# Optimization experiments

Hardware: AMD Instinct MI355X
Metric: run time of the kernel (lower is better)

## Reference

```python
import jax, jax.numpy as jnp
import numpy as np

B, C, H, W_SP = 32, 128, 56, 56
OC, K, STRIDE, PAD = 256, 3, 1, 1


def setup_inputs() -> dict:
    key = jax.random.key(0)
    k1, k2, k3 = jax.random.split(key, 3)
    x = jax.random.normal(k1, (B, C, H, W_SP), dtype=jnp.float32)
    # nn.Linear weight: [out_features, in_features] = [OC, C*K*K]
    W = jax.random.normal(k2, (OC, C * K * K), dtype=jnp.float32) * 0.02
    b = jax.random.normal(k3, (OC,), dtype=jnp.float32) * 0.02
    return {"x": x, "W": W, "b": b}


def reference(x, W, b):
    # The torch module does im2col (unfold+permute+reshape) then Linear.
    # Patch layout after view/permute is (C, kh, kw) flattened, so the
    # Linear weight reshaped to [OC, C, K, K] is exactly an OIHW conv
    # kernel; direct convolution computes identical math without
    # materializing the im2col tensor.
    kernel = W.reshape(OC, C, K, K)
    out = jax.lax.conv_general_dilated(
        x, kernel,
        window_strides=(STRIDE, STRIDE),
        padding=[(PAD, PAD), (PAD, PAD)],
        dimension_numbers=("NCHW", "OIHW", "NCHW"),
    )
    return out + b[None, :, None, None]
```

## Files before the change

kernel.cpp:

```cpp
#include <hip/hip_runtime.h>
#include <hip/hip_bf16.h>
#include <stdint.h>

typedef unsigned short u16;
typedef unsigned int   u32;
typedef __bf16 bf16x8 __attribute__((ext_vector_type(8)));
typedef float  f32x4  __attribute__((ext_vector_type(4)));

#define BATCH 32
#define CIN   128
#define HH    56
#define WW    56
#define OC    256
#define HP    58
#define WP    58
#define PLANE  (HH*WW)
#define KDIM   1152
#define NKT    36

#define XPAD_ELEMS (BATCH*HP*WP*CIN)
#define W3_ELEMS   (OC*KDIM)

#define GLDS16(g, l) __builtin_amdgcn_global_load_lds( \
    (const __attribute__((address_space(1))) void*)(g), \
    (__attribute__((address_space(3))) void*)(l), 16, 0, 0)

__global__ void zero_border(uint4* __restrict__ xp4) {
    int i = blockIdx.x * 256 + threadIdx.x;
    if (i >= 64 * 928) return;
    int row = i / 928;
    int off = i - row * 928;
    int b = row >> 1;
    int h = (row & 1) ? (HP - 1) : 0;
    xp4[((size_t)(b * HP + h) * WP * CIN) / 8 + off] = (uint4){0, 0, 0, 0};
}

__global__ __launch_bounds__(256) void pad_tr(const float* __restrict__ x,
                                              u16* __restrict__ xpad) {
    __shared__ u16 T16[56 * 130];
    const int h = blockIdx.x;
    const int b = blockIdx.y;
    const int tid = threadIdx.x;

    const float* src = x + (size_t)b * CIN * PLANE + h * WW;
#pragma unroll
    for (int j = 0; j < 28; ++j) {
        int flat = j * 256 + tid;
        int c = flat / 56;
        int w = flat - c * 56;
        float v = src[(size_t)c * PLANE + w];
        __hip_bfloat16 bv = __float2bfloat16(v);
        T16[w * 130 + c] = *(u16*)&bv;
    }
    __syncthreads();

    const u32* T32 = (const u32*)T16;
    uint4* dst = (uint4*)(xpad + (size_t)(b * HP + h + 1) * WP * CIN);
#pragma unroll
    for (int j = 0; j < 4; ++j) {
        int g = j * 256 + tid;
        if (g < 928) {
            int wp = g >> 4, cq = g & 15;
            uint4 v = (uint4){0, 0, 0, 0};
            if (wp >= 1 && wp <= 56) {
                int w = wp - 1;
                v.x = T32[w * 65 + cq * 4 + 0];
                v.y = T32[w * 65 + cq * 4 + 1];
                v.z = T32[w * 65 + cq * 4 + 2];
                v.w = T32[w * 65 + cq * 4 + 3];
            }
            dst[g] = v;
        }
    }
}

__global__ void pack_w(const float* __restrict__ W, u16* __restrict__ w3) {
    int o = blockIdx.x * blockDim.x + threadIdx.x;
    if (o >= W3_ELEMS) return;
    int nt   = o / (NKT * 4096);
    int rem  = o - nt * (NKT * 4096);
    int kt   = rem / 4096;
    int rem2 = rem - kt * 4096;
    int ni   = rem2 >> 5;
    int ci   = rem2 & 31;
    int n = nt * 128 + ni;
    int r = kt >> 2;
    int c = ((kt & 3) << 5) + ci;
    float val = W[n * KDIM + c * 9 + r];
    __hip_bfloat16 bv = __float2bfloat16(val);
    w3[o] = *(u16*)&bv;
}

__global__ __launch_bounds__(256) void conv_main(
    const u16* __restrict__ xpad,
    const u16* __restrict__ w3,
    const float* __restrict__ bias,
    float* __restrict__ out)
{
    __shared__ __align__(16) u16 As[2][128 * 32];
    __shared__ __align__(16) u16 Bs[2][128 * 32];

    const int tid  = threadIdx.x;
    const int lane = tid & 63;
    const int wv   = tid >> 6;
    const int m0   = blockIdx.x * 128;
    const int nt   = blockIdx.y;

    const int srow = lane >> 2;
    const int sc   = lane & 3;
    size_t abase[2], bbase[2];
#pragma unroll
    for (int i = 0; i < 2; ++i) {
        int rowid = wv * 32 + i * 16 + srow;
        int q = (sc - ((rowid >> 1) & 3)) & 3;
        abase[i] = (size_t)rowid * 64 + q * 16;
        int m  = m0 + rowid;
        int bb = m / PLANE;
        int s  = m - bb * PLANE;
        int hh = s / WW;
        int ww = s - hh * WW;
        bbase[i] = ((size_t)((bb * HP + hh) * WP + ww) * CIN) * 2 + q * 16;
    }
    const char* w3t = (const char*)(w3 + (size_t)nt * (NKT * 4096));
    const char* xb  = (const char*)xpad;
    char* AsW[2] = { (char*)As[0] + wv * 2048, (char*)As[1] + wv * 2048 };
    char* BsW[2] = { (char*)Bs[0] + wv * 2048, (char*)Bs[1] + wv * 2048 };

    const int wn = wv >> 1, wm = wv & 1;
    const int l16 = lane & 15, quad = lane >> 4;

    int aoff[4], boff[4];
#pragma unroll
    for (int f = 0; f < 4; ++f) {
        int ra = wn * 64 + f * 16 + l16;
        aoff[f] = ra * 64 + ((quad + (ra >> 1)) & 3) * 16;
        int rb = wm * 64 + f * 16 + l16;
        boff[f] = rb * 64 + ((quad + (rb >> 1)) & 3) * 16;
    }

    f32x4 acc[4][4];
#pragma unroll
    for (int f = 0; f < 4; ++f) {
        f32x4 bv = *(const f32x4*)&bias[nt * 128 + wn * 64 + f * 16 + quad * 4];
#pragma unroll
        for (int g = 0; g < 4; ++g) acc[f][g] = bv;
    }

    auto issue = [&](int kt) {
        const int buf = kt & 1;
        const int r  = kt >> 2;
        const int cc = kt & 3;
        const int kh = r / 3;
        const int kw = r - kh * 3;
        const size_t xoff = ((size_t)(kh * WP + kw) * CIN + cc * 32) * 2;
#pragma unroll
        for (int i = 0; i < 2; ++i) {
            GLDS16(w3t + (size_t)kt * 8192 + abase[i], AsW[buf] + i * 1024);
            GLDS16(xb + bbase[i] + xoff,               BsW[buf] + i * 1024);
        }
    };

    issue(0);
#pragma unroll
    for (int kt = 0; kt < NKT; ++kt) {
        __syncthreads();
        if (kt + 1 < NKT) issue(kt + 1);

        const char* Ab = (const char*)As[kt & 1];
        const char* Bb = (const char*)Bs[kt & 1];
        bf16x8 af[4], bfr[4];
#pragma unroll
        for (int f = 0; f < 4; ++f)
            af[f] = *(const bf16x8*)(Ab + aoff[f]);
#pragma unroll
        for (int g = 0; g < 4; ++g)
            bfr[g] = *(const bf16x8*)(Bb + boff[g]);

#pragma unroll
        for (int f = 0; f < 4; ++f)
#pragma unroll
            for (int g = 0; g < 4; ++g)
                acc[f][g] = __builtin_amdgcn_mfma_f32_16x16x32_bf16(
                    af[f], bfr[g], acc[f][g], 0, 0, 0);
    }

    const int n0 = nt * 128 + wn * 64;
#pragma unroll
    for (int g = 0; g < 4; ++g) {
        const int mm = m0 + wm * 64 + g * 16 + l16;
        const int bb = mm / PLANE;
        const int ss = mm - bb * PLANE;
        float* obase = out + (size_t)bb * (OC * PLANE) + ss;
#pragma unroll
        for (int f = 0; f < 4; ++f) {
#pragma unroll
            for (int i = 0; i < 4; ++i) {
                const int n = n0 + f * 16 + quad * 4 + i;
                obase[(size_t)n * PLANE] = acc[f][g][i];
            }
        }
    }
}

extern "C" void kernel_launch(void* const* d_in, const int* in_sizes, int n_in,
                              void* d_out, int out_size, void* d_ws, size_t ws_size,
                              hipStream_t stream) {
    const float* x    = (const float*)d_in[0];
    const float* W    = (const float*)d_in[1];
    const float* bias = (const float*)d_in[2];
    float* out = (float*)d_out;

    u16* xpad = (u16*)d_ws;
    u16* w3   = xpad + XPAD_ELEMS;

    zero_border<<<232, 256, 0, stream>>>((uint4*)xpad);
    pad_tr<<<dim3(HH, BATCH), 256, 0, stream>>>(x, xpad);
    pack_w<<<(W3_ELEMS + 255) / 256, 256, 0, stream>>>(W, w3);

    dim3 grid(784, 2);
    conv_main<<<grid, 256, 0, stream>>>(xpad, w3, bias, out);
}
```

Measured before the change: 217.1 us.

## Enlarge conv GEMM tile to 256x256 with K=64 steps and staged ping-pong pipeline

The implicit-GEMM convolution moves from 128x128 tiles with K=32 steps to 256(M)x256(N) tiles with K=64 steps, using 8 waves per block and 392 blocks. The weight packing is rewritten into a matching swizzled layout. The main loop splits each K step into four MFMA quadrants, with interleaved async global-to-LDS staging, explicit barriers, waitcnt control and setprio, which should improve data reuse and overlap loads with compute. Block IDs are also remapped to spread tiles. The risks are higher register and LDS pressure and fewer blocks than the CU count for good occupancy.

```diff
diff --git a/kernel.cpp b/kernel.cpp
--- a/kernel.cpp
+++ b/kernel.cpp
@@ -16,7 +16,7 @@
 #define WP    58
 #define PLANE  (HH*WW)
 #define KDIM   1152
-#define NKT    36
+#define NT     18
 
 #define XPAD_ELEMS (BATCH*HP*WP*CIN)
 #define W3_ELEMS   (OC*KDIM)
@@ -77,127 +77,216 @@
 __global__ void pack_w(const float* __restrict__ W, u16* __restrict__ w3) {
     int o = blockIdx.x * blockDim.x + threadIdx.x;
     if (o >= W3_ELEMS) return;
-    int nt   = o / (NKT * 4096);
-    int rem  = o - nt * (NKT * 4096);
-    int kt   = rem / 4096;
-    int rem2 = rem - kt * 4096;
-    int ni   = rem2 >> 5;
-    int ci   = rem2 & 31;
-    int n = nt * 128 + ni;
-    int r = kt >> 2;
-    int c = ((kt & 3) << 5) + ci;
-    float val = W[n * KDIM + c * 9 + r];
+    int T   = o >> 14;
+    int rem = o & 16383;
+    int oc  = rem >> 6;
+    int kk  = rem & 63;
+    int p   = kk >> 3;
+    int e   = kk & 7;
+    int rot = ((oc & 127) >> 1) & 7;
+    int c64 = ((p - rot) & 7) * 8 + e;
+    int r   = T >> 1;
+    int c128 = (T & 1) * 64 + c64;
+    float val = W[oc * KDIM + c128 * 9 + r];
     __hip_bfloat16 bv = __float2bfloat16(val);
     w3[o] = *(u16*)&bv;
 }
 
-__global__ __launch_bounds__(256) void conv_main(
+__global__ __launch_bounds__(512, 2) void conv_main(
     const u16* __restrict__ xpad,
     const u16* __restrict__ w3,
     const float* __restrict__ bias,
     float* __restrict__ out)
 {
-    __shared__ __align__(16) u16 As[2][128 * 32];
-    __shared__ __align__(16) u16 Bs[2][128 * 32];
+    __shared__ __align__(16) u16 WL[2 * 2 * 128 * 64];
+    __shared__ __align__(16) u16 XL[2 * 2 * 128 * 64];
 
     const int tid  = threadIdx.x;
     const int lane = tid & 63;
     const int wv   = tid >> 6;
-    const int m0   = blockIdx.x * 128;
-    const int nt   = blockIdx.y;
-
-    const int srow = lane >> 2;
-    const int sc   = lane & 3;
-    size_t abase[2], bbase[2];
-#pragma unroll
-    for (int i = 0; i < 2; ++i) {
-        int rowid = wv * 32 + i * 16 + srow;
-        int q = (sc - ((rowid >> 1) & 3)) & 3;
-        abase[i] = (size_t)rowid * 64 + q * 16;
-        int m  = m0 + rowid;
-        int bb = m / PLANE;
-        int s  = m - bb * PLANE;
-        int hh = s / WW;
-        int ww = s - hh * WW;
-        bbase[i] = ((size_t)((bb * HP + hh) * WP + ww) * CIN) * 2 + q * 16;
-    }
-    const char* w3t = (const char*)(w3 + (size_t)nt * (NKT * 4096));
+    const int wm   = wv >> 2;
+    const int wn   = wv & 3;
+    const int l16  = lane & 15;
+    const int quad = lane >> 4;
+
+    const int bid  = blockIdx.x;
+    const int tile = (bid & 7) * 49 + (bid >> 3);
+    const int m0   = tile * 256;
+
+    const int srow8 = lane >> 3;
+    const int spos  = lane & 7;
+    size_t xsrc[2][2];
+#pragma unroll
+    for (int h = 0; h < 2; ++h)
+#pragma unroll
+        for (int i = 0; i < 2; ++i) {
+            int r  = (wv * 2 + i) * 8 + srow8;
+            int q  = (spos - ((r >> 1) & 7)) & 7;
+            int m  = m0 + h * 128 + r;
+            int b  = m / PLANE;
+            int s  = m - b * PLANE;
+            int hh = s / WW;
+            int ww = s - hh * WW;
+            xsrc[h][i] = ((size_t)((b * HP + hh) * WP + ww) * CIN) * 2 + (size_t)q * 16;
+        }
     const char* xb  = (const char*)xpad;
-    char* AsW[2] = { (char*)As[0] + wv * 2048, (char*)As[1] + wv * 2048 };
-    char* BsW[2] = { (char*)Bs[0] + wv * 2048, (char*)Bs[1] + wv * 2048 };
-
-    const int wn = wv >> 1, wm = wv & 1;
-    const int l16 = lane & 15, quad = lane >> 4;
-
-    int aoff[4], boff[4];
+    const char* w3b = (const char*)w3;
+    const int dstat     = wv * 2048;
+    const int wsrc_lane = wv * 2048 + lane * 16;
+
+    auto xkoff = [&](int kt) -> int {
+        int r9 = kt >> 1;
+        int kh = (r9 * 11) >> 5;
+        int kw = r9 - kh * 3;
+        return ((kh * WP + kw) * CIN + (kt & 1) * 64) * 2;
+    };
+    auto stageW = [&](int kt, int h) {
+        const char* src = w3b + (size_t)kt * 32768 + h * 16384 + wsrc_lane;
+        char* dst = (char*)WL + (kt & 1) * 32768 + h * 16384 + dstat;
+        GLDS16(src,        dst);
+        GLDS16(src + 1024, dst + 1024);
+    };
+    auto stageX = [&](int kt, int h, int xko) {
+        char* dst = (char*)XL + (kt & 1) * 32768 + h * 16384 + dstat;
+        GLDS16(xb + xsrc[h][0] + xko, dst);
+        GLDS16(xb + xsrc[h][1] + xko, dst + 1024);
+    };
+
+    int woff[2], xoff[4];
+#pragma unroll
+    for (int j = 0; j < 2; ++j) {
+        int r = wn * 32 + j * 16 + l16;
+        woff[j] = r * 128 + (((quad + (r >> 1)) & 7) << 4);
+    }
+#pragma unroll
+    for (int j = 0; j < 4; ++j) {
+        int r = wm * 64 + j * 16 + l16;
+        xoff[j] = r * 128 + (((quad + (r >> 1)) & 7) << 4);
+    }
+
+    f32x4 acc[4][8];
 #pragma unroll
     for (int f = 0; f < 4; ++f) {
-        int ra = wn * 64 + f * 16 + l16;
-        aoff[f] = ra * 64 + ((quad + (ra >> 1)) & 3) * 16;
-        int rb = wm * 64 + f * 16 + l16;
-        boff[f] = rb * 64 + ((quad + (rb >> 1)) & 3) * 16;
-    }
-
-    f32x4 acc[4][4];
-#pragma unroll
-    for (int f = 0; f < 4; ++f) {
-        f32x4 bv = *(const f32x4*)&bias[nt * 128 + wn * 64 + f * 16 + quad * 4];
-#pragma unroll
-        for (int g = 0; g < 4; ++g) acc[f][g] = bv;
-    }
-
-    auto issue = [&](int kt) {
-        const int buf = kt & 1;
-        const int r  = kt >> 2;
-        const int cc = kt & 3;
-        const int kh = r / 3;
-        const int kw = r - kh * 3;
-        const size_t xoff = ((size_t)(kh * WP + kw) * CIN + cc * 32) * 2;
-#pragma unroll
-        for (int i = 0; i < 2; ++i) {
-            GLDS16(w3t + (size_t)kt * 8192 + abase[i], AsW[buf] + i * 1024);
-            GLDS16(xb + bbase[i] + xoff,               BsW[buf] + i * 1024);
-        }
-    };
-
-    issue(0);
-#pragma unroll
-    for (int kt = 0; kt < NKT; ++kt) {
-        __syncthreads();
-        if (kt + 1 < NKT) issue(kt + 1);
-
-        const char* Ab = (const char*)As[kt & 1];
-        const char* Bb = (const char*)Bs[kt & 1];
-        bf16x8 af[4], bfr[4];
-#pragma unroll
-        for (int f = 0; f < 4; ++f)
-            af[f] = *(const bf16x8*)(Ab + aoff[f]);
-#pragma unroll
-        for (int g = 0; g < 4; ++g)
-            bfr[g] = *(const bf16x8*)(Bb + boff[g]);
-
-#pragma unroll
-        for (int f = 0; f < 4; ++f)
+        const int ob = (f >> 1) * 128 + wn * 32 + (f & 1) * 16 + quad * 4;
+        f32x4 bv = *(const f32x4*)&bias[ob];
+#pragma unroll
+        for (int g = 0; g < 8; ++g) acc[f][g] = bv;
+    }
+
+    stageW(0, 0); stageW(0, 1);
+    stageX(0, 0, xkoff(0)); stageX(0, 1, xkoff(0));
+    stageW(1, 0); stageX(1, 0, xkoff(1)); stageW(1, 1);
+    asm volatile("s_waitcnt vmcnt(6)" ::: "memory");
+    __builtin_amdgcn_sched_barrier(0);
+    __builtin_amdgcn_s_barrier();
+
+#pragma unroll 1
+    for (int kt = 0; kt < NT; ++kt) {
+        const char* Wb = (const char*)WL + (kt & 1) * 32768;
+        const char* Xb = (const char*)XL + (kt & 1) * 32768;
+        const bool st2 = (kt + 2 < NT);
+
+        bf16x8 wlo[2][2], xlo[4][2];
+#pragma unroll
+        for (int j = 0; j < 2; ++j) {
+            wlo[j][0] = *(const bf16x8*)(Wb + woff[j]);
+            wlo[j][1] = *(const bf16x8*)(Wb + (woff[j] ^ 64));
+        }
+#pragma unroll
+        for (int j = 0; j < 4; ++j) {
+            xlo[j][0] = *(const bf16x8*)(Xb + xoff[j]);
+            xlo[j][1] = *(const bf16x8*)(Xb + (xoff[j] ^ 64));
+        }
+        if (kt + 1 < NT) stageX(kt + 1, 1, xkoff(kt + 1));
+        __builtin_amdgcn_s_barrier();
+        asm volatile("s_waitcnt lgkmcnt(0)" ::: "memory");
+        __builtin_amdgcn_sched_barrier(0);
+        __builtin_amdgcn_s_setprio(1);
+#pragma unroll
+        for (int f = 0; f < 2; ++f)
 #pragma unroll
             for (int g = 0; g < 4; ++g)
-                acc[f][g] = __builtin_amdgcn_mfma_f32_16x16x32_bf16(
-                    af[f], bfr[g], acc[f][g], 0, 0, 0);
-    }
-
-    const int n0 = nt * 128 + wn * 64;
-#pragma unroll
-    for (int g = 0; g < 4; ++g) {
-        const int mm = m0 + wm * 64 + g * 16 + l16;
+#pragma unroll
+                for (int s = 0; s < 2; ++s)
+                    acc[f][g] = __builtin_amdgcn_mfma_f32_16x16x32_bf16(
+                        wlo[f][s], xlo[g][s], acc[f][g], 0, 0, 0);
+        __builtin_amdgcn_s_setprio(0);
+        __builtin_amdgcn_s_barrier();
+
+        bf16x8 whi[2][2];
+#pragma unroll
+        for (int j = 0; j < 2; ++j) {
+            whi[j][0] = *(const bf16x8*)(Wb + 16384 + woff[j]);
+            whi[j][1] = *(const bf16x8*)(Wb + 16384 + (woff[j] ^ 64));
+        }
+        if (st2) stageW(kt + 2, 0);
+        __builtin_amdgcn_s_barrier();
+        asm volatile("s_waitcnt lgkmcnt(0)" ::: "memory");
+        __builtin_amdgcn_sched_barrier(0);
+        __builtin_amdgcn_s_setprio(1);
+#pragma unroll
+        for (int f = 0; f < 2; ++f)
+#pragma unroll
+            for (int g = 0; g < 4; ++g)
+#pragma unroll
+                for (int s = 0; s < 2; ++s)
+                    acc[2 + f][g] = __builtin_amdgcn_mfma_f32_16x16x32_bf16(
+                        whi[f][s], xlo[g][s], acc[2 + f][g], 0, 0, 0);
+        __builtin_amdgcn_s_setprio(0);
+        __builtin_amdgcn_s_barrier();
+
+        bf16x8 xhi[4][2];
+#pragma unroll
+        for (int j = 0; j < 4; ++j) {
+            xhi[j][0] = *(const bf16x8*)(Xb + 16384 + xoff[j]);
+            xhi[j][1] = *(const bf16x8*)(Xb + 16384 + (xoff[j] ^ 64));
+        }
+        if (st2) stageX(kt + 2, 0, xkoff(kt + 2));
+        __builtin_amdgcn_s_barrier();
+        asm volatile("s_waitcnt lgkmcnt(0)" ::: "memory");
+        __builtin_amdgcn_sched_barrier(0);
+        __builtin_amdgcn_s_setprio(1);
+#pragma unroll
+        for (int f = 0; f < 2; ++f)
+#pragma unroll
+            for (int g = 0; g < 4; ++g)
+#pragma unroll
+                for (int s = 0; s < 2; ++s)
+                    acc[f][4 + g] = __builtin_amdgcn_mfma_f32_16x16x32_bf16(
+                        wlo[f][s], xhi[g][s], acc[f][4 + g], 0, 0, 0);
+        __builtin_amdgcn_s_setprio(0);
+        __builtin_amdgcn_s_barrier();
+
+        if (st2) stageW(kt + 2, 1);
+        __builtin_amdgcn_s_barrier();
+        __builtin_amdgcn_s_setprio(1);
+#pragma unroll
+        for (int f = 0; f < 2; ++f)
+#pragma unroll
+            for (int g = 0; g < 4; ++g)
+#pragma unroll
+                for (int s = 0; s < 2; ++s)
+                    acc[2 + f][4 + g] = __builtin_amdgcn_mfma_f32_16x16x32_bf16(
+                        whi[f][s], xhi[g][s], acc[2 + f][4 + g], 0, 0, 0);
+        __builtin_amdgcn_s_setprio(0);
+        if (kt < NT - 2) asm volatile("s_waitcnt vmcnt(6)" ::: "memory");
+        else             asm volatile("s_waitcnt vmcnt(0)" ::: "memory");
+        __builtin_amdgcn_sched_barrier(0);
+        __builtin_amdgcn_s_barrier();
+    }
+
+#pragma unroll
+    for (int g = 0; g < 8; ++g) {
+        const int mm = m0 + (g >> 2) * 128 + wm * 64 + (g & 3) * 16 + l16;
         const int bb = mm / PLANE;
         const int ss = mm - bb * PLANE;
         float* obase = out + (size_t)bb * (OC * PLANE) + ss;
 #pragma unroll
         for (int f = 0; f < 4; ++f) {
-#pragma unroll
-            for (int i = 0; i < 4; ++i) {
-                const int n = n0 + f * 16 + quad * 4 + i;
-                obase[(size_t)n * PLANE] = acc[f][g][i];
-            }
+            const int n = (f >> 1) * 128 + wn * 32 + (f & 1) * 16 + quad * 4;
+#pragma unroll
+            for (int i = 0; i < 4; ++i)
+                obase[(size_t)(n + i) * PLANE] = acc[f][g][i];
         }
     }
 }
@@ -217,6 +306,5 @@
     pad_tr<<<dim3(HH, BATCH), 256, 0, stream>>>(x, xpad);
     pack_w<<<(W3_ELEMS + 255) / 256, 256, 0, stream>>>(W, w3);
 
-    dim3 grid(784, 2);
-    conv_main<<<grid, 256, 0, stream>>>(xpad, w3, bias, out);
-}
+    conv_main<<<392, 512, 0, stream>>>(xpad, w3, bias, out);
+}
```

New measurement: 224.1 us. 1.03x slower.

## Compute all 256 output channels per block and remap tiles across XCDs

Applied to the files above, without the earlier changes.

The conv GEMM block tile grows from 128x128 to 256 output channels by 128 pixels, so each block loads the padded input tile once instead of twice across two channel-tile blocks. The weight pack layout is changed to pre-apply the LDS swizzle, tiles are remapped so neighbouring pixel tiles land on the same XCD, MFMA sections get raised wave priority, and the main loop is no longer unrolled. The pad/transpose kernel reads float2 pairs. Accumulators double to 128 floats per thread, which raises register pressure and may cost occupancy despite the launch-bounds hint.

```diff
diff --git a/kernel.cpp b/kernel.cpp
--- a/kernel.cpp
+++ b/kernel.cpp
@@ -16,7 +16,7 @@
 #define WP    58
 #define PLANE  (HH*WW)
 #define KDIM   1152
-#define NKT    36
+#define NT     36
 
 #define XPAD_ELEMS (BATCH*HP*WP*CIN)
 #define W3_ELEMS   (OC*KDIM)
@@ -44,13 +44,16 @@
 
     const float* src = x + (size_t)b * CIN * PLANE + h * WW;
 #pragma unroll
-    for (int j = 0; j < 28; ++j) {
+    for (int j = 0; j < 14; ++j) {
         int flat = j * 256 + tid;
-        int c = flat / 56;
-        int w = flat - c * 56;
-        float v = src[(size_t)c * PLANE + w];
-        __hip_bfloat16 bv = __float2bfloat16(v);
-        T16[w * 130 + c] = *(u16*)&bv;
+        int c  = flat / 28;
+        int wp = flat - c * 28;
+        int w  = wp * 2;
+        float2 v = *(const float2*)&src[(size_t)c * PLANE + w];
+        __hip_bfloat16 b0 = __float2bfloat16(v.x);
+        __hip_bfloat16 b1 = __float2bfloat16(v.y);
+        T16[w * 130 + c]       = *(u16*)&b0;
+        T16[(w + 1) * 130 + c] = *(u16*)&b1;
     }
     __syncthreads();
 
@@ -77,127 +80,135 @@
 __global__ void pack_w(const float* __restrict__ W, u16* __restrict__ w3) {
     int o = blockIdx.x * blockDim.x + threadIdx.x;
     if (o >= W3_ELEMS) return;
-    int nt   = o / (NKT * 4096);
-    int rem  = o - nt * (NKT * 4096);
-    int kt   = rem / 4096;
-    int rem2 = rem - kt * 4096;
-    int ni   = rem2 >> 5;
-    int ci   = rem2 & 31;
-    int n = nt * 128 + ni;
-    int r = kt >> 2;
-    int c = ((kt & 3) << 5) + ci;
-    float val = W[n * KDIM + c * 9 + r];
+    int T   = o >> 13;
+    int rem = o & 8191;
+    int oc  = rem >> 5;
+    int kk  = rem & 31;
+    int p   = kk >> 3;
+    int e   = kk & 7;
+    int rot = (oc >> 1) & 3;
+    int c32 = ((p - rot) & 3) * 8 + e;
+    int r   = T >> 2;
+    int c128 = (T & 3) * 32 + c32;
+    float val = W[oc * KDIM + c128 * 9 + r];
     __hip_bfloat16 bv = __float2bfloat16(val);
     w3[o] = *(u16*)&bv;
 }
 
-__global__ __launch_bounds__(256) void conv_main(
+__global__ __launch_bounds__(256, 2) void conv_main(
     const u16* __restrict__ xpad,
     const u16* __restrict__ w3,
     const float* __restrict__ bias,
     float* __restrict__ out)
 {
-    __shared__ __align__(16) u16 As[2][128 * 32];
-    __shared__ __align__(16) u16 Bs[2][128 * 32];
+    __shared__ __align__(16) u16 WL[2][256 * 32];
+    __shared__ __align__(16) u16 XL[2][128 * 32];
 
     const int tid  = threadIdx.x;
     const int lane = tid & 63;
     const int wv   = tid >> 6;
-    const int m0   = blockIdx.x * 128;
-    const int nt   = blockIdx.y;
-
-    const int srow = lane >> 2;
-    const int sc   = lane & 3;
-    size_t abase[2], bbase[2];
+    const int l16  = lane & 15;
+    const int quad = lane >> 4;
+
+    const int bid  = blockIdx.x;
+    const int tile = (bid & 7) * 98 + (bid >> 3);
+    const int m0   = tile * 128;
+
+    const int srow = tid >> 2;
+    const int spos = tid & 3;
+    size_t xsrc[2];
 #pragma unroll
     for (int i = 0; i < 2; ++i) {
-        int rowid = wv * 32 + i * 16 + srow;
-        int q = (sc - ((rowid >> 1) & 3)) & 3;
-        abase[i] = (size_t)rowid * 64 + q * 16;
-        int m  = m0 + rowid;
-        int bb = m / PLANE;
-        int s  = m - bb * PLANE;
+        int r  = i * 64 + srow;
+        int q  = (spos - ((r >> 1) & 3)) & 3;
+        int m  = m0 + r;
+        int b  = m / PLANE;
+        int s  = m - b * PLANE;
         int hh = s / WW;
         int ww = s - hh * WW;
-        bbase[i] = ((size_t)((bb * HP + hh) * WP + ww) * CIN) * 2 + q * 16;
-    }
-    const char* w3t = (const char*)(w3 + (size_t)nt * (NKT * 4096));
+        xsrc[i] = ((size_t)((b * HP + hh) * WP + ww) * CIN) * 2 + (size_t)q * 16;
+    }
     const char* xb  = (const char*)xpad;
-    char* AsW[2] = { (char*)As[0] + wv * 2048, (char*)As[1] + wv * 2048 };
-    char* BsW[2] = { (char*)Bs[0] + wv * 2048, (char*)Bs[1] + wv * 2048 };
-
-    const int wn = wv >> 1, wm = wv & 1;
-    const int l16 = lane & 15, quad = lane >> 4;
-
-    int aoff[4], boff[4];
-#pragma unroll
-    for (int f = 0; f < 4; ++f) {
-        int ra = wn * 64 + f * 16 + l16;
-        aoff[f] = ra * 64 + ((quad + (ra >> 1)) & 3) * 16;
-        int rb = wm * 64 + f * 16 + l16;
-        boff[f] = rb * 64 + ((quad + (rb >> 1)) & 3) * 16;
-    }
-
-    f32x4 acc[4][4];
-#pragma unroll
-    for (int f = 0; f < 4; ++f) {
-        f32x4 bv = *(const f32x4*)&bias[nt * 128 + wn * 64 + f * 16 + quad * 4];
-#pragma unroll
-        for (int g = 0; g < 4; ++g) acc[f][g] = bv;
-    }
-
+    const char* w3b = (const char*)w3;
+
+    auto xkoff = [&](int kt) -> int {
+        int r9 = kt >> 2;
+        int kh = (r9 * 11) >> 5;
+        int kw = r9 - kh * 3;
+        return ((kh * WP + kw) * CIN + (kt & 3) * 32) * 2;
+    };
     auto issue = [&](int kt) {
         const int buf = kt & 1;
-        const int r  = kt >> 2;
-        const int cc = kt & 3;
-        const int kh = r / 3;
-        const int kw = r - kh * 3;
-        const size_t xoff = ((size_t)(kh * WP + kw) * CIN + cc * 32) * 2;
-#pragma unroll
-        for (int i = 0; i < 2; ++i) {
-            GLDS16(w3t + (size_t)kt * 8192 + abase[i], AsW[buf] + i * 1024);
-            GLDS16(xb + bbase[i] + xoff,               BsW[buf] + i * 1024);
-        }
+        const char* wsrc = w3b + (size_t)kt * 16384 + tid * 16;
+        char* wdst = (char*)WL[buf] + tid * 16;
+#pragma unroll
+        for (int j = 0; j < 4; ++j)
+            GLDS16(wsrc + j * 4096, wdst + j * 4096);
+        const int xko = xkoff(kt);
+        char* xdst = (char*)XL[buf] + tid * 16;
+#pragma unroll
+        for (int i = 0; i < 2; ++i)
+            GLDS16(xb + xsrc[i] + xko, xdst + i * 4096);
     };
 
+    int woff[4], xoff[8];
+#pragma unroll
+    for (int f = 0; f < 4; ++f) {
+        int r = wv * 64 + f * 16 + l16;
+        woff[f] = r * 64 + (((quad + (r >> 1)) & 3) << 4);
+    }
+#pragma unroll
+    for (int g = 0; g < 8; ++g) {
+        int r = g * 16 + l16;
+        xoff[g] = r * 64 + (((quad + (r >> 1)) & 3) << 4);
+    }
+
+    f32x4 acc[4][8];
+#pragma unroll
+    for (int f = 0; f < 4; ++f) {
+        f32x4 bv = *(const f32x4*)&bias[wv * 64 + f * 16 + quad * 4];
+#pragma unroll
+        for (int g = 0; g < 8; ++g) acc[f][g] = bv;
+    }
+
     issue(0);
-#pragma unroll
-    for (int kt = 0; kt < NKT; ++kt) {
+#pragma unroll 1
+    for (int kt = 0; kt < NT; ++kt) {
         __syncthreads();
-        if (kt + 1 < NKT) issue(kt + 1);
-
-        const char* Ab = (const char*)As[kt & 1];
-        const char* Bb = (const char*)Bs[kt & 1];
-        bf16x8 af[4], bfr[4];
+        if (kt + 1 < NT) issue(kt + 1);
+
+        const char* Wb = (const char*)WL[kt & 1];
+        const char* Xb = (const char*)XL[kt & 1];
+        bf16x8 wf[4], xf[8];
 #pragma unroll
         for (int f = 0; f < 4; ++f)
-            af[f] = *(const bf16x8*)(Ab + aoff[f]);
-#pragma unroll
-        for (int g = 0; g < 4; ++g)
-            bfr[g] = *(const bf16x8*)(Bb + boff[g]);
-
+            wf[f] = *(const bf16x8*)(Wb + woff[f]);
+#pragma unroll
+        for (int g = 0; g < 8; ++g)
+            xf[g] = *(const bf16x8*)(Xb + xoff[g]);
+
+        __builtin_amdgcn_s_setprio(1);
 #pragma unroll
         for (int f = 0; f < 4; ++f)
 #pragma unroll
-            for (int g = 0; g < 4; ++g)
+            for (int g = 0; g < 8; ++g)
                 acc[f][g] = __builtin_amdgcn_mfma_f32_16x16x32_bf16(
-                    af[f], bfr[g], acc[f][g], 0, 0, 0);
-    }
-
-    const int n0 = nt * 128 + wn * 64;
-#pragma unroll
-    for (int g = 0; g < 4; ++g) {
-        const int mm = m0 + wm * 64 + g * 16 + l16;
+                    wf[f], xf[g], acc[f][g], 0, 0, 0);
+        __builtin_amdgcn_s_setprio(0);
+    }
+
+#pragma unroll
+    for (int g = 0; g < 8; ++g) {
+        const int mm = m0 + g * 16 + l16;
         const int bb = mm / PLANE;
         const int ss = mm - bb * PLANE;
         float* obase = out + (size_t)bb * (OC * PLANE) + ss;
 #pragma unroll
         for (int f = 0; f < 4; ++f) {
-#pragma unroll
-            for (int i = 0; i < 4; ++i) {
-                const int n = n0 + f * 16 + quad * 4 + i;
-                obase[(size_t)n * PLANE] = acc[f][g][i];
-            }
+            const int n = wv * 64 + f * 16 + quad * 4;
+#pragma unroll
+            for (int i = 0; i < 4; ++i)
+                obase[(size_t)(n + i) * PLANE] = acc[f][g][i];
         }
     }
 }
@@ -217,6 +228,5 @@
     pad_tr<<<dim3(HH, BATCH), 256, 0, stream>>>(x, xpad);
     pack_w<<<(W3_ELEMS + 255) / 256, 256, 0, stream>>>(W, w3);
 
-    dim3 grid(784, 2);
-    conv_main<<<grid, 256, 0, stream>>>(xpad, w3, bias, out);
-}
+    conv_main<<<784, 256, 0, stream>>>(xpad, w3, bias, out);
+}
```

Result: no change. 216.8 us (-0.1%).
